# Kernel optimization log

Hardware: AMD Instinct MI355X
Metric: run time of the kernel (lower is better)

Reference implementation:

```python
import jax, jax.numpy as jnp
import numpy as np

NUM_CLASSES = 1000
NUM_NEIGHBOURS = 200
SIGMA = 10.0
GAUSS_CONST = 1.0 / (2.0 * SIGMA ** 2)


def setup_inputs() -> dict:
    key = jax.random.key(0)
    k1, k2, k3 = jax.random.split(key, 3)
    B, D, C = 512, 512, 100000
    features = jax.random.normal(k1, (B, D), dtype=jnp.float32)
    centres = jax.random.normal(k2, (C, D), dtype=jnp.float32)
    centre_labels = jax.random.randint(k3, (C,), 0, NUM_CLASSES)
    weight = jnp.zeros((C,), dtype=jnp.float32)
    return {"features": features, "centres": centres,
            "centre_labels": centre_labels, "weight": weight}


def _knn(features, centres, k):
    # squared euclidean distances [B, C] without materializing [B, C, D]
    f2 = jnp.sum(features * features, axis=1, keepdims=True)      # [B,1]
    c2 = jnp.sum(centres * centres, axis=1)                        # [C]
    d2 = f2 + c2[None, :] - 2.0 * features @ centres.T             # [B,C]
    _, idx = jax.lax.top_k(-d2, k)                                 # smallest k
    return idx                                                     # [B,k]


def reference(features, centres, centre_labels, weight):
    B = features.shape[0]
    K = NUM_NEIGHBOURS
    nbr = _knn(features, centres, K)                               # [B,K] int
    gathered = centres[nbr]                                        # [B,K,D]
    d2 = jnp.sum((features[:, None, :] - gathered) ** 2, axis=-1)  # [B,K]
    kernel_weights = jnp.exp(weight)                               # [C]
    d = jnp.exp(-d2 * GAUSS_CONST) * kernel_weights[nbr]           # [B,K]
    nbr_labels = centre_labels[nbr]                                # [B,K]
    rows = jnp.arange(B)[:, None]
    p = jnp.zeros((B, NUM_CLASSES), dtype=d.dtype).at[rows, nbr_labels].add(d)
    p = jnp.where(p == 0, 1e-10, p)
    p = p / jnp.sum(p, axis=1, keepdims=True)
    return jnp.log(p)
```

## Files before the change

### kernel.cpp

```cpp
#include <hip/hip_runtime.h>
#include <hip/hip_fp16.h>
#include <math.h>
#include <stdint.h>

#define D_DIM    512
#define NCLS     1000
#define KSEL     200
#define NBINS    1024
#define HREP     4
#define CAND_MAX 2048
#define GCONST   0.005
#define MARGIN   2.0f

typedef short s8v __attribute__((ext_vector_type(8)));
typedef float f4v __attribute__((ext_vector_type(4)));

#define GLOAD_LDS16(gp, lp) __builtin_amdgcn_global_load_lds( \
    (const __attribute__((address_space(1))) void*)(gp),      \
    (__attribute__((address_space(3))) void*)(lp), 16, 0, 0)

static __device__ __forceinline__ unsigned short f2bf(float x) {
    unsigned u = __float_as_uint(x);
    return (unsigned short)((u + 0x7FFFu + ((u >> 16) & 1u)) >> 16);
}

static __device__ __forceinline__ unsigned cvt_pk_bf16(float lo, float hi) {
    unsigned r;
    asm("v_cvt_pk_bf16_f32 %0, %1, %2" : "=v"(r) : "v"(lo), "v"(hi));
    return r;
}

__global__ __launch_bounds__(256)
void convertF(const float* __restrict__ F, unsigned short* __restrict__ Fb,
              float* __restrict__ f2)
{
    __shared__ float red[256];
    const int r = blockIdx.x, t = threadIdx.x;
    float2 v = *(const float2*)(F + (size_t)r * D_DIM + t * 2);
    ushort2 o; o.x = f2bf(v.x); o.y = f2bf(v.y);
    *(ushort2*)(Fb + (size_t)r * D_DIM + t * 2) = o;
    red[t] = v.x * v.x + v.y * v.y;
    __syncthreads();
    for (int off = 128; off > 0; off >>= 1) {
        if (t < off) red[t] += red[t + off];
        __syncthreads();
    }
    if (t == 0) f2[r] = red[0];
}

__global__ __launch_bounds__(256)
void convertC(const float* __restrict__ C, unsigned short* __restrict__ Cb,
              float* __restrict__ c2, int N)
{
    const int wv = threadIdx.x >> 6, lane = threadIdx.x & 63;
    const int stride = gridDim.x * 4;
    for (int r = blockIdx.x * 4 + wv; r < N; r += stride) {
        const float* rp = C + (size_t)r * D_DIM + lane * 8;
        float4 a = *(const float4*)rp;
        float4 b = *(const float4*)(rp + 4);
        uint4 o;
        o.x = cvt_pk_bf16(a.x, a.y);
        o.y = cvt_pk_bf16(a.z, a.w);
        o.z = cvt_pk_bf16(b.x, b.y);
        o.w = cvt_pk_bf16(b.z, b.w);
        *(uint4*)(Cb + (size_t)r * D_DIM + lane * 8) = o;
        float s = a.x*a.x + a.y*a.y + a.z*a.z + a.w*a.w
                + b.x*b.x + b.y*b.y + b.z*b.z + b.w*b.w;
        s += __shfl_xor(s, 1, 64);
        s += __shfl_xor(s, 2, 64);
        s += __shfl_xor(s, 4, 64);
        s += __shfl_xor(s, 8, 64);
        s += __shfl_xor(s, 16, 64);
        s += __shfl_xor(s, 32, 64);
        if (lane == 0) c2[r] = s;
    }
}

__global__ __launch_bounds__(256)
void mfma_gemm_pure(const unsigned short* __restrict__ Fb,
                    const unsigned short* __restrict__ Cb,
                    __half* __restrict__ Sm, int N)
{
    __shared__ short smem[2 * 128 * 64];
    short* As = smem;
    short* Bs = smem + 128 * 64;
    const int t    = threadIdx.x;
    const int lane = t & 63;
    const int w    = t >> 6;
    const int wm   = w >> 1, wn = w & 1;
    const int m0   = blockIdx.x * 128;
    const int n0   = blockIdx.y * 128;
    const int lrow = lane >> 3;
    const int oct  = (lane & 7) ^ lrow;
    const int quad = lane >> 4;
    const int col  = lane & 15;

    f4v acc[4][4];
#pragma unroll
    for (int i = 0; i < 4; ++i)
#pragma unroll
        for (int j = 0; j < 4; ++j) acc[i][j] = (f4v){0.f, 0.f, 0.f, 0.f};

    for (int k0 = 0; k0 < D_DIM; k0 += 64) {
        __syncthreads();
#pragma unroll
        for (int cc = 0; cc < 4; ++cc) {
            int ch = w * 4 + cc;
            GLOAD_LDS16(Fb + (size_t)(m0 + ch * 8 + lrow) * D_DIM + k0 + oct * 8,
                        &As[ch * 512]);
        }
#pragma unroll
        for (int cc = 0; cc < 4; ++cc) {
            int ch = w * 4 + cc;
            int rg = n0 + ch * 8 + lrow;
            rg = rg < N ? rg : N - 1;
            GLOAD_LDS16(Cb + (size_t)rg * D_DIM + k0 + oct * 8,
                        &Bs[ch * 512]);
        }
        __syncthreads();

#pragma unroll
        for (int kk = 0; kk < 2; ++kk) {
            s8v a[4], b[4];
#pragma unroll
            for (int i = 0; i < 4; ++i) {
                int row  = wm * 64 + i * 16 + col;
                int slot = (kk * 4 + quad) ^ (col & 7);
                a[i] = *(s8v*)&As[row * 64 + slot * 8];
            }
#pragma unroll
            for (int j = 0; j < 4; ++j) {
                int row  = wn * 64 + j * 16 + col;
                int slot = (kk * 4 + quad) ^ (col & 7);
                b[j] = *(s8v*)&Bs[row * 64 + slot * 8];
            }
#pragma unroll
            for (int i = 0; i < 4; ++i)
#pragma unroll
                for (int j = 0; j < 4; ++j)
                    acc[i][j] = __builtin_amdgcn_mfma_f32_16x16x32_bf16(
                        a[i], b[j], acc[i][j], 0, 0, 0);
        }
    }

    __syncthreads();
    __half* Cs = (__half*)smem;
#pragma unroll
    for (int i = 0; i < 4; ++i) {
#pragma unroll
        for (int j = 0; j < 4; ++j) {
#pragma unroll
            for (int v = 0; v < 4; ++v) {
                int ml = wm * 64 + i * 16 + quad * 4 + v;
                int nl = wn * 64 + j * 16 + col;
                int slot = ((nl >> 3) ^ (ml & 7));
                Cs[ml * 128 + slot * 8 + (nl & 7)] = __float2half(acc[i][j][v]);
            }
        }
    }
    __syncthreads();
#pragma unroll
    for (int it = 0; it < 8; ++it) {
        int idx = it * 256 + t;
        int row = idx >> 4;
        int o8  = idx & 15;
        int n   = n0 + o8 * 8;
        const __half* src = &Cs[row * 128 + ((o8 ^ (row & 7)) * 8)];
        __half* dst = Sm + (size_t)(m0 + row) * N + n;
        if (n + 7 < N) {
            *(uint4*)dst = *(const uint4*)src;
        } else if (n < N) {
            for (int e = 0; e < 8 && n + e < N; ++e) dst[e] = src[e];
        }
    }
}

__global__ __launch_bounds__(256)
void mfma_gemm_fused(const unsigned short* __restrict__ Fb,
                     const float* __restrict__ C,
                     float* __restrict__ c2g,
                     __half* __restrict__ Sm, int N)
{
    __shared__ short smem[2 * 128 * 64];
    short* As = smem;
    short* Bs = smem + 128 * 64;
    const int t    = threadIdx.x;
    const int lane = t & 63;
    const int w    = t >> 6;
    const int wm   = w >> 1, wn = w & 1;
    const int m0   = blockIdx.x * 128;
    const int n0   = blockIdx.y * 128;
    const int lrow = lane >> 3;
    const int oct  = (lane & 7) ^ lrow;
    const int quad = lane >> 4;
    const int col  = lane & 15;

    f4v acc[4][4];
#pragma unroll
    for (int i = 0; i < 4; ++i)
#pragma unroll
        for (int j = 0; j < 4; ++j) acc[i][j] = (f4v){0.f, 0.f, 0.f, 0.f};

    float  c2part[4] = {0.f, 0.f, 0.f, 0.f};
    float4 ra[4], rb[4];

#pragma unroll
    for (int cc = 0; cc < 4; ++cc) {
        int row = (w * 4 + cc) * 8 + lrow;
        int rg  = n0 + row; rg = rg < N ? rg : N - 1;
        const float* gp = C + (size_t)rg * D_DIM + oct * 8;
        ra[cc] = *(const float4*)gp;
        rb[cc] = *(const float4*)(gp + 4);
    }

    for (int k0 = 0; k0 < D_DIM; k0 += 64) {
        __syncthreads();
#pragma unroll
        for (int cc = 0; cc < 4; ++cc) {
            int ch = w * 4 + cc;
            GLOAD_LDS16(Fb + (size_t)(m0 + ch * 8 + lrow) * D_DIM + k0 + oct * 8,
                        &As[ch * 512]);
        }
#pragma unroll
        for (int cc = 0; cc < 4; ++cc) {
            int row = (w * 4 + cc) * 8 + lrow;
            float4 va = ra[cc], vb = rb[cc];
            c2part[cc] += va.x*va.x + va.y*va.y + va.z*va.z + va.w*va.w
                        + vb.x*vb.x + vb.y*vb.y + vb.z*vb.z + vb.w*vb.w;
            uint4 o;
            o.x = cvt_pk_bf16(va.x, va.y);
            o.y = cvt_pk_bf16(va.z, va.w);
            o.z = cvt_pk_bf16(vb.x, vb.y);
            o.w = cvt_pk_bf16(vb.z, vb.w);
            *(uint4*)&Bs[row * 64 + (lane & 7) * 8] = o;
        }
        __syncthreads();

        if (k0 + 64 < D_DIM) {
#pragma unroll
            for (int cc = 0; cc < 4; ++cc) {
                int row = (w * 4 + cc) * 8 + lrow;
                int rg  = n0 + row; rg = rg < N ? rg : N - 1;
                const float* gp = C + (size_t)rg * D_DIM + (k0 + 64) + oct * 8;
                ra[cc] = *(const float4*)gp;
                rb[cc] = *(const float4*)(gp + 4);
            }
        }

#pragma unroll
        for (int kk = 0; kk < 2; ++kk) {
            s8v a[4], b[4];
#pragma unroll
            for (int i = 0; i < 4; ++i) {
                int row  = wm * 64 + i * 16 + col;
                int slot = (kk * 4 + quad) ^ (col & 7);
                a[i] = *(s8v*)&As[row * 64 + slot * 8];
            }
#pragma unroll
            for (int j = 0; j < 4; ++j) {
                int row  = wn * 64 + j * 16 + col;
                int slot = (kk * 4 + quad) ^ (col & 7);
                b[j] = *(s8v*)&Bs[row * 64 + slot * 8];
            }
#pragma unroll
            for (int i = 0; i < 4; ++i)
#pragma unroll
                for (int j = 0; j < 4; ++j)
                    acc[i][j] = __builtin_amdgcn_mfma_f32_16x16x32_bf16(
                        a[i], b[j], acc[i][j], 0, 0, 0);
        }
    }

#pragma unroll
    for (int cc = 0; cc < 4; ++cc) {
        float s = c2part[cc];
        s += __shfl_xor(s, 1, 64);
        s += __shfl_xor(s, 2, 64);
        s += __shfl_xor(s, 4, 64);
        int row = (w * 4 + cc) * 8 + lrow;
        if (m0 == 0 && (lane & 7) == 0 && (n0 + row) < N)
            c2g[n0 + row] = s;
    }

    __syncthreads();
    __half* Cs = (__half*)smem;
#pragma unroll
    for (int i = 0; i < 4; ++i) {
#pragma unroll
        for (int j = 0; j < 4; ++j) {
#pragma unroll
            for (int v = 0; v < 4; ++v) {
                int ml = wm * 64 + i * 16 + quad * 4 + v;
                int nl = wn * 64 + j * 16 + col;
                int slot = ((nl >> 3) ^ (ml & 7));
                Cs[ml * 128 + slot * 8 + (nl & 7)] = __float2half(acc[i][j][v]);
            }
        }
    }
    __syncthreads();
#pragma unroll
    for (int it = 0; it < 8; ++it) {
        int idx = it * 256 + t;
        int row = idx >> 4;
        int o8  = idx & 15;
        int n   = n0 + o8 * 8;
        const __half* src = &Cs[row * 128 + ((o8 ^ (row & 7)) * 8)];
        __half* dst = Sm + (size_t)(m0 + row) * N + n;
        if (n + 7 < N) {
            *(uint4*)dst = *(const uint4*)src;
        } else if (n < N) {
            for (int e = 0; e < 8 && n + e < N; ++e) dst[e] = src[e];
        }
    }
}

__global__ __launch_bounds__(1024)
void fused_select(const __half* __restrict__ Sm, const float* __restrict__ f2,
                  const float* __restrict__ c2,
                  const float* __restrict__ F, const float* __restrict__ C,
                  const int* __restrict__ labels, const float* __restrict__ weight,
                  float* __restrict__ out, int N)
{
    __shared__ unsigned hist[NBINS * HREP];
    __shared__ float    fs[D_DIM];
    __shared__ int      idxs[CAND_MAX];
    __shared__ double   dists[CAND_MAX];
    __shared__ float    p[NCLS];
    __shared__ float    red[1024];
    __shared__ unsigned scanbuf[256];
    __shared__ float    sT;
    __shared__ unsigned scnt;

    const int r = blockIdx.x, t = threadIdx.x;
    for (int b = t; b < NBINS * HREP; b += 1024) hist[b] = 0u;
    for (int c = t; c < NCLS; c += 1024) p[c] = 0.f;
    for (int k = t; k < D_DIM; k += 1024) fs[k] = F[(size_t)r * D_DIM + k];
    if (t == 0) { sT = 1e30f; scnt = 0u; }
    __syncthreads();

    const float fr = f2[r];
    const __half* srow = Sm + (size_t)r * N;

    for (int j = t * 8; j < N; j += 8192) {
        uint4 sv = *(const uint4*)(srow + j);
        float4 ca = *(const float4*)(c2 + j);
        float4 cb = *(const float4*)(c2 + j + 4);
        float2 s0 = __half22float2(*(__half2*)&sv.x);
        float2 s1 = __half22float2(*(__half2*)&sv.y);
        float2 s2 = __half22float2(*(__half2*)&sv.z);
        float2 s3 = __half22float2(*(__half2*)&sv.w);
        float d2v[8] = { fr + ca.x - 2.f * s0.x, fr + ca.y - 2.f * s0.y,
                         fr + ca.z - 2.f * s1.x, fr + ca.w - 2.f * s1.y,
                         fr + cb.x - 2.f * s2.x, fr + cb.y - 2.f * s2.y,
                         fr + cb.z - 2.f * s3.x, fr + cb.w - 2.f * s3.y };
#pragma unroll
        for (int e = 0; e < 8; ++e) {
            int b = (int)(d2v[e] * 0.5f);
            b = b < 0 ? 0 : (b > NBINS - 1 ? NBINS - 1 : b);
            atomicAdd(&hist[(b << 2) + (t & 3)], 1u);
        }
    }
    __syncthreads();

    if (t < 256) {
        unsigned loc[NBINS / 256];
        unsigned s = 0;
#pragma unroll
        for (int i = 0; i < NBINS / 256; ++i) {
            int bb = t * (NBINS / 256) + i;
            loc[i] = hist[(bb << 2) + 0] + hist[(bb << 2) + 1]
                   + hist[(bb << 2) + 2] + hist[(bb << 2) + 3];
            s += loc[i];
        }
        scanbuf[t] = s;
        __syncthreads();
        unsigned pre = 0;
        for (int u = 0; u < t; ++u) pre += scanbuf[u];
        if (pre < KSEL && pre + s >= KSEL) {
            unsigned cum = pre;
            int b = NBINS - 1;
#pragma unroll
            for (int i = 0; i < NBINS / 256; ++i) {
                cum += loc[i];
                if (cum >= KSEL) { b = t * (NBINS / 256) + i; break; }
            }
            sT = 2.0f * (float)(b + 1) + MARGIN;
        }
    } else {
        __syncthreads();
    }
    __syncthreads();
    const float Tr = sT;

    for (int j = t * 8; j < N; j += 8192) {
        uint4 sv = *(const uint4*)(srow + j);
        float4 ca = *(const float4*)(c2 + j);
        float4 cb = *(const float4*)(c2 + j + 4);
        float2 s0 = __half22float2(*(__half2*)&sv.x);
        float2 s1 = __half22float2(*(__half2*)&sv.y);
        float2 s2 = __half22float2(*(__half2*)&sv.z);
        float2 s3 = __half22float2(*(__half2*)&sv.w);
        float d2v[8] = { fr + ca.x - 2.f * s0.x, fr + ca.y - 2.f * s0.y,
                         fr + ca.z - 2.f * s1.x, fr + ca.w - 2.f * s1.y,
                         fr + cb.x - 2.f * s2.x, fr + cb.y - 2.f * s2.y,
                         fr + cb.z - 2.f * s3.x, fr + cb.w - 2.f * s3.y };
#pragma unroll
        for (int e = 0; e < 8; ++e) {
            if (d2v[e] <= Tr) {
                unsigned pos = atomicAdd(&scnt, 1u);
                if (pos < CAND_MAX) idxs[pos] = j + e;
            }
        }
    }
    __syncthreads();
    int Nc = (int)scnt;
    if (Nc > CAND_MAX) Nc = CAND_MAX;

    {
        const int wv = t >> 6, lane = t & 63;
        for (int i = wv; i < Nc; i += 16) {
            int ci = idxs[i];
            const float* cp = C + (size_t)ci * D_DIM;
            float4 a  = *(const float4*)(cp + lane * 8);
            float4 b  = *(const float4*)(cp + lane * 8 + 4);
            float4 fa = *(const float4*)(fs + lane * 8);
            float4 fb = *(const float4*)(fs + lane * 8 + 4);
            double d0 = (double)fa.x - (double)a.x;
            double d1 = (double)fa.y - (double)a.y;
            double d2 = (double)fa.z - (double)a.z;
            double d3 = (double)fa.w - (double)a.w;
            double d4 = (double)fb.x - (double)b.x;
            double d5 = (double)fb.y - (double)b.y;
            double d6 = (double)fb.z - (double)b.z;
            double d7 = (double)fb.w - (double)b.w;
            double acc = d0*d0 + d1*d1 + d2*d2 + d3*d3
                       + d4*d4 + d5*d5 + d6*d6 + d7*d7;
#pragma unroll
            for (int off = 32; off > 0; off >>= 1)
                acc += __shfl_down(acc, off, 64);
            if (lane == 0) dists[i] = acc;
        }
    }
    __syncthreads();

    int ksel = KSEL < Nc ? KSEL : Nc;
    for (int i = t; i < Nc; i += 1024) {
        double di = dists[i];
        int    ii = idxs[i];
        int rank = 0;
        for (int j = 0; j < Nc; ++j) {
            double dj = dists[j];
            rank += (dj < di) || (dj == di && idxs[j] < ii);
        }
        if (rank < ksel) {
            double wgt = exp(-di * GCONST) * exp((double)weight[ii]);
            atomicAdd(&p[labels[ii]], (float)wgt);
        }
    }
    __syncthreads();

    float s = 0.f;
    for (int c = t; c < NCLS; c += 1024) {
        float v = p[c];
        if (v == 0.f) v = 1e-10f;
        p[c] = v;
        s += v;
    }
    red[t] = s;
    __syncthreads();
    for (int o = 512; o > 0; o >>= 1) {
        if (t < o) red[t] += red[t + o];
        __syncthreads();
    }
    float total = red[0];
    for (int c = t; c < NCLS; c += 1024)
        out[(size_t)r * NCLS + c] = logf(p[c] / total);
}

extern "C" void kernel_launch(void* const* d_in, const int* in_sizes, int n_in,
                              void* d_out, int out_size, void* d_ws, size_t ws_size,
                              hipStream_t stream)
{
    const float* features = (const float*)d_in[0];
    const float* centres  = (const float*)d_in[1];
    const int*   labels   = (const int*)d_in[2];
    const float* weight   = (const float*)d_in[3];
    const int B = in_sizes[0] / D_DIM;
    const int N = in_sizes[2];
    float* out = (float*)d_out;

    uint8_t* w = (uint8_t*)d_ws;
    size_t off = 0;
    auto alloc = [&](size_t bytes) -> uint8_t* {
        uint8_t* ptr = w + off;
        off = (off + bytes + 255) & ~(size_t)255;
        return ptr;
    };
    float*          f2 = (float*)alloc((size_t)B * 4);
    float*          c2 = (float*)alloc((size_t)N * 4);
    unsigned short* Fb = (unsigned short*)alloc((size_t)B * D_DIM * 2);
    __half*         Sm = (__half*)alloc((size_t)B * N * 2);

    const size_t need_cb = off + (size_t)N * D_DIM * 2;
    const bool   full    = ws_size >= need_cb;

    convertF<<<B, 256, 0, stream>>>(features, Fb, f2);

    if (full) {
        unsigned short* Cb = (unsigned short*)alloc((size_t)N * D_DIM * 2);
        convertC<<<2048, 256, 0, stream>>>(centres, Cb, c2, N);
        dim3 ggrid(B / 128, (N + 127) / 128);
        mfma_gemm_pure<<<ggrid, 256, 0, stream>>>(Fb, Cb, Sm, N);
    } else {
        dim3 ggrid(B / 128, (N + 127) / 128);
        mfma_gemm_fused<<<ggrid, 256, 0, stream>>>(Fb, centres, c2, Sm, N);
    }

    fused_select<<<B, 1024, 0, stream>>>(Sm, f2, c2, features, centres,
                                         labels, weight, out, N);
}
```

Baseline: 490.8 us.

## Fuse distance epilogue into GEMM with 256-row tiles and store fp16 d2

```diff
diff --git a/kernel.cpp b/kernel.cpp
--- a/kernel.cpp
+++ b/kernel.cpp
@@ -10,7 +10,7 @@
 #define HREP     4
 #define CAND_MAX 2048
 #define GCONST   0.005
-#define MARGIN   2.0f
+#define MARGIN   4.0f
 
 typedef short s8v __attribute__((ext_vector_type(8)));
 typedef float f4v __attribute__((ext_vector_type(4)));
@@ -76,19 +76,21 @@
     }
 }
 
-__global__ __launch_bounds__(256)
+__global__ __launch_bounds__(512)
 void mfma_gemm_pure(const unsigned short* __restrict__ Fb,
                     const unsigned short* __restrict__ Cb,
-                    __half* __restrict__ Sm, int N)
+                    const float* __restrict__ f2,
+                    const float* __restrict__ c2,
+                    __half* __restrict__ Dm, int N)
 {
-    __shared__ short smem[2 * 128 * 64];
+    __shared__ short smem[32 * 512 + 16 * 512];
     short* As = smem;
-    short* Bs = smem + 128 * 64;
+    short* Bs = smem + 32 * 512;
     const int t    = threadIdx.x;
     const int lane = t & 63;
     const int w    = t >> 6;
     const int wm   = w >> 1, wn = w & 1;
-    const int m0   = blockIdx.x * 128;
+    const int m0   = blockIdx.x * 256;
     const int n0   = blockIdx.y * 128;
     const int lrow = lane >> 3;
     const int oct  = (lane & 7) ^ lrow;
@@ -110,8 +112,8 @@
                         &As[ch * 512]);
         }
 #pragma unroll
-        for (int cc = 0; cc < 4; ++cc) {
-            int ch = w * 4 + cc;
+        for (int cc = 0; cc < 2; ++cc) {
+            int ch = w * 2 + cc;
             int rg = n0 + ch * 8 + lrow;
             rg = rg < N ? rg : N - 1;
             GLOAD_LDS16(Cb + (size_t)rg * D_DIM + k0 + oct * 8,
@@ -121,56 +123,74 @@
 
 #pragma unroll
         for (int kk = 0; kk < 2; ++kk) {
-            s8v a[4], b[4];
+            int slot = (kk * 4 + quad) ^ (col & 7);
+            s8v b[4];
+#pragma unroll
+            for (int j = 0; j < 4; ++j) {
+                int row = wn * 64 + j * 16 + col;
+                b[j] = *(s8v*)&Bs[row * 64 + slot * 8];
+            }
 #pragma unroll
             for (int i = 0; i < 4; ++i) {
-                int row  = wm * 64 + i * 16 + col;
-                int slot = (kk * 4 + quad) ^ (col & 7);
-                a[i] = *(s8v*)&As[row * 64 + slot * 8];
-            }
-#pragma unroll
-            for (int j = 0; j < 4; ++j) {
-                int row  = wn * 64 + j * 16 + col;
-                int slot = (kk * 4 + quad) ^ (col & 7);
-                b[j] = *(s8v*)&Bs[row * 64 + slot * 8];
-            }
-#pragma unroll
-            for (int i = 0; i < 4; ++i)
+                int row = wm * 64 + i * 16 + col;
+                s8v a = *(s8v*)&As[row * 64 + slot * 8];
 #pragma unroll
                 for (int j = 0; j < 4; ++j)
                     acc[i][j] = __builtin_amdgcn_mfma_f32_16x16x32_bf16(
-                        a[i], b[j], acc[i][j], 0, 0, 0);
-        }
-    }
-
-    __syncthreads();
+                        a, b[j], acc[i][j], 0, 0, 0);
+            }
+        }
+    }
+
+    float c2v[4];
+#pragma unroll
+    for (int j = 0; j < 4; ++j) {
+        int idx = n0 + wn * 64 + j * 16 + col;
+        idx = idx < N ? idx : N - 1;
+        c2v[j] = c2[idx];
+    }
+    float fv[4][4];
+#pragma unroll
+    for (int i = 0; i < 4; ++i)
+#pragma unroll
+        for (int v = 0; v < 4; ++v)
+            fv[i][v] = f2[m0 + wm * 64 + i * 16 + quad * 4 + v];
+
     __half* Cs = (__half*)smem;
 #pragma unroll
-    for (int i = 0; i < 4; ++i) {
-#pragma unroll
-        for (int j = 0; j < 4; ++j) {
-#pragma unroll
-            for (int v = 0; v < 4; ++v) {
-                int ml = wm * 64 + i * 16 + quad * 4 + v;
-                int nl = wn * 64 + j * 16 + col;
-                int slot = ((nl >> 3) ^ (ml & 7));
-                Cs[ml * 128 + slot * 8 + (nl & 7)] = __float2half(acc[i][j][v]);
-            }
-        }
-    }
-    __syncthreads();
-#pragma unroll
-    for (int it = 0; it < 8; ++it) {
-        int idx = it * 256 + t;
-        int row = idx >> 4;
-        int o8  = idx & 15;
-        int n   = n0 + o8 * 8;
-        const __half* src = &Cs[row * 128 + ((o8 ^ (row & 7)) * 8)];
-        __half* dst = Sm + (size_t)(m0 + row) * N + n;
-        if (n + 7 < N) {
-            *(uint4*)dst = *(const uint4*)src;
-        } else if (n < N) {
-            for (int e = 0; e < 8 && n + e < N; ++e) dst[e] = src[e];
+    for (int h = 0; h < 2; ++h) {
+        __syncthreads();
+        if ((wm >> 1) == h) {
+            int mlb = (wm & 1) * 64;
+#pragma unroll
+            for (int i = 0; i < 4; ++i) {
+#pragma unroll
+                for (int j = 0; j < 4; ++j) {
+#pragma unroll
+                    for (int v = 0; v < 4; ++v) {
+                        int ml = mlb + i * 16 + quad * 4 + v;
+                        int nl = wn * 64 + j * 16 + col;
+                        float d2 = fv[i][v] + c2v[j] - 2.f * acc[i][j][v];
+                        int slot = (nl >> 3) ^ (ml & 7);
+                        Cs[ml * 128 + slot * 8 + (nl & 7)] = __float2half(d2);
+                    }
+                }
+            }
+        }
+        __syncthreads();
+#pragma unroll
+        for (int it = 0; it < 4; ++it) {
+            int idx = it * 512 + t;
+            int row = idx >> 4;
+            int o8  = idx & 15;
+            int n   = n0 + o8 * 8;
+            const __half* src = &Cs[row * 128 + ((o8 ^ (row & 7)) * 8)];
+            __half* dst = Dm + (size_t)(m0 + h * 128 + row) * N + n;
+            if (n + 7 < N) {
+                *(uint4*)dst = *(const uint4*)src;
+            } else if (n < N) {
+                for (int e = 0; e < 8 && n + e < N; ++e) dst[e] = src[e];
+            }
         }
     }
 }
@@ -319,7 +339,7 @@
                   const float* __restrict__ c2,
                   const float* __restrict__ F, const float* __restrict__ C,
                   const int* __restrict__ labels, const float* __restrict__ weight,
-                  float* __restrict__ out, int N)
+                  float* __restrict__ out, int N, int d2mode)
 {
     __shared__ unsigned hist[NBINS * HREP];
     __shared__ float    fs[D_DIM];
@@ -343,16 +363,22 @@
 
     for (int j = t * 8; j < N; j += 8192) {
         uint4 sv = *(const uint4*)(srow + j);
-        float4 ca = *(const float4*)(c2 + j);
-        float4 cb = *(const float4*)(c2 + j + 4);
         float2 s0 = __half22float2(*(__half2*)&sv.x);
         float2 s1 = __half22float2(*(__half2*)&sv.y);
         float2 s2 = __half22float2(*(__half2*)&sv.z);
         float2 s3 = __half22float2(*(__half2*)&sv.w);
-        float d2v[8] = { fr + ca.x - 2.f * s0.x, fr + ca.y - 2.f * s0.y,
-                         fr + ca.z - 2.f * s1.x, fr + ca.w - 2.f * s1.y,
-                         fr + cb.x - 2.f * s2.x, fr + cb.y - 2.f * s2.y,
-                         fr + cb.z - 2.f * s3.x, fr + cb.w - 2.f * s3.y };
+        float d2v[8];
+        if (d2mode) {
+            d2v[0]=s0.x; d2v[1]=s0.y; d2v[2]=s1.x; d2v[3]=s1.y;
+            d2v[4]=s2.x; d2v[5]=s2.y; d2v[6]=s3.x; d2v[7]=s3.y;
+        } else {
+            float4 ca = *(const float4*)(c2 + j);
+            float4 cb = *(const float4*)(c2 + j + 4);
+            d2v[0]=fr+ca.x-2.f*s0.x; d2v[1]=fr+ca.y-2.f*s0.y;
+            d2v[2]=fr+ca.z-2.f*s1.x; d2v[3]=fr+ca.w-2.f*s1.y;
+            d2v[4]=fr+cb.x-2.f*s2.x; d2v[5]=fr+cb.y-2.f*s2.y;
+            d2v[6]=fr+cb.z-2.f*s3.x; d2v[7]=fr+cb.w-2.f*s3.y;
+        }
 #pragma unroll
         for (int e = 0; e < 8; ++e) {
             int b = (int)(d2v[e] * 0.5f);
@@ -394,16 +420,22 @@
 
     for (int j = t * 8; j < N; j += 8192) {
         uint4 sv = *(const uint4*)(srow + j);
-        float4 ca = *(const float4*)(c2 + j);
-        float4 cb = *(const float4*)(c2 + j + 4);
         float2 s0 = __half22float2(*(__half2*)&sv.x);
         float2 s1 = __half22float2(*(__half2*)&sv.y);
         float2 s2 = __half22float2(*(__half2*)&sv.z);
         float2 s3 = __half22float2(*(__half2*)&sv.w);
-        float d2v[8] = { fr + ca.x - 2.f * s0.x, fr + ca.y - 2.f * s0.y,
-                         fr + ca.z - 2.f * s1.x, fr + ca.w - 2.f * s1.y,
-                         fr + cb.x - 2.f * s2.x, fr + cb.y - 2.f * s2.y,
-                         fr + cb.z - 2.f * s3.x, fr + cb.w - 2.f * s3.y };
+        float d2v[8];
+        if (d2mode) {
+            d2v[0]=s0.x; d2v[1]=s0.y; d2v[2]=s1.x; d2v[3]=s1.y;
+            d2v[4]=s2.x; d2v[5]=s2.y; d2v[6]=s3.x; d2v[7]=s3.y;
+        } else {
+            float4 ca = *(const float4*)(c2 + j);
+            float4 cb = *(const float4*)(c2 + j + 4);
+            d2v[0]=fr+ca.x-2.f*s0.x; d2v[1]=fr+ca.y-2.f*s0.y;
+            d2v[2]=fr+ca.z-2.f*s1.x; d2v[3]=fr+ca.w-2.f*s1.y;
+            d2v[4]=fr+cb.x-2.f*s2.x; d2v[5]=fr+cb.y-2.f*s2.y;
+            d2v[6]=fr+cb.z-2.f*s3.x; d2v[7]=fr+cb.w-2.f*s3.y;
+        }
 #pragma unroll
         for (int e = 0; e < 8; ++e) {
             if (d2v[e] <= Tr) {
@@ -508,14 +540,14 @@
 
     if (full) {
         unsigned short* Cb = (unsigned short*)alloc((size_t)N * D_DIM * 2);
-        convertC<<<2048, 256, 0, stream>>>(centres, Cb, c2, N);
-        dim3 ggrid(B / 128, (N + 127) / 128);
-        mfma_gemm_pure<<<ggrid, 256, 0, stream>>>(Fb, Cb, Sm, N);
+        convertC<<<4096, 256, 0, stream>>>(centres, Cb, c2, N);
+        dim3 ggrid(B / 256, (N + 127) / 128);
+        mfma_gemm_pure<<<ggrid, 512, 0, stream>>>(Fb, Cb, f2, c2, Sm, N);
     } else {
         dim3 ggrid(B / 128, (N + 127) / 128);
         mfma_gemm_fused<<<ggrid, 256, 0, stream>>>(Fb, centres, c2, Sm, N);
     }
 
     fused_select<<<B, 1024, 0, stream>>>(Sm, f2, c2, features, centres,
-                                         labels, weight, out, N);
-}
+                                         labels, weight, out, N, full ? 1 : 0);
+}
```

After: 504.0 us. +2.7%, slower.
